# Performance work log

Measured on AMD Instinct MI355X. Metric: run time of the kernel, lower is better.

The kernel has to match this reference:

```python
import jax, jax.numpy as jnp
import numpy as np

NUM_EMBEDDINGS = 512
EMBEDDING_DIM = 64
COMMITMENT_COST = 0.25


def setup_inputs() -> dict:
    key = jax.random.key(0)
    k1, k2 = jax.random.split(key)
    inputs = jax.random.normal(k1, (128, 1024, EMBEDDING_DIM), dtype=jnp.float32)
    embedding = jax.random.normal(k2, (NUM_EMBEDDINGS, EMBEDDING_DIM), dtype=jnp.float32)
    return {"inputs": inputs, "embedding": embedding}


def reference(inputs, embedding):
    """Eval-mode forward of VectorQuantizerEMA.

    Returns (loss, quantized, perplexity, encodings), matching the torch module
    with self.training == False.
    """
    input_shape = inputs.shape
    flat = inputs.reshape(-1, EMBEDDING_DIM)                      # [N, D]
    distances = (
        jnp.sum(flat ** 2, axis=1, keepdims=True)
        + jnp.sum(embedding ** 2, axis=1)
        - 2.0 * flat @ embedding.T
    )
    encoding_indices = jnp.argmin(distances, axis=1)              # [N]
    encodings = jax.nn.one_hot(encoding_indices, NUM_EMBEDDINGS, dtype=jnp.float32)  # [N, K]
    # quantized = onehot @ W  ==  gather rows (same math, cheaper)
    quantized = jnp.take(embedding, encoding_indices, axis=0).reshape(input_shape)

    e_latent_loss = jnp.mean((jax.lax.stop_gradient(quantized) - inputs) ** 2)
    loss = COMMITMENT_COST * e_latent_loss

    # straight-through estimator
    quantized = inputs + jax.lax.stop_gradient(quantized - inputs)

    avg_probs = jnp.mean(encodings, axis=0)                       # [K]
    perplexity = jnp.exp(-jnp.sum(avg_probs * jnp.log(avg_probs + 1e-10)))
    return loss, quantized, perplexity, encodings
```

## Files before the change

### kernel.cpp

```cpp
#include <hip/hip_runtime.h>
#include <math.h>


#define NK 512
#define ND 64
#define NROWS 131072
#define ROWS_PB 64
#define BLOCK 256
#define NBLOCKS (NROWS / ROWS_PB)
#define NTILES 32
#define XSTRIDE 68
#define MARGIN 0.02f

#define Q_OFF    1
#define PERP_OFF 8388609
#define ENC_OFF  8388610

typedef float vf2 __attribute__((ext_vector_type(2)));
typedef float vf4 __attribute__((ext_vector_type(4)));
typedef short vs8 __attribute__((ext_vector_type(8)));

__device__ __forceinline__ unsigned short bf16_rne(float v) {
    union { float f; unsigned int u; } a; a.f = v;
    return (unsigned short)((a.u + 0x7FFFu + ((a.u >> 16) & 1u)) >> 16);
}
__device__ __forceinline__ float bf16_to_f(unsigned short s) {
    union { unsigned int u; float f; } a; a.u = ((unsigned int)s) << 16;
    return a.f;
}

__global__ __launch_bounds__(64) void vq_prep(const float* __restrict__ emb,
                                              float* __restrict__ eknorm,
                                              unsigned int* __restrict__ efrag) {
    const int t = blockIdx.x;
    const int l = threadIdx.x;
    const int c = t * 16 + (l & 15);
    const int quad = l >> 4;
    #pragma unroll
    for (int f = 0; f < 4; ++f) {
        const int kbase = (f & 1) * 32 + quad * 8;
        unsigned int w[4];
        #pragma unroll
        for (int d = 0; d < 4; ++d) {
            float v0 = emb[c * ND + kbase + 2 * d];
            float v1 = emb[c * ND + kbase + 2 * d + 1];
            unsigned short h0 = bf16_rne(v0), h1 = bf16_rne(v1);
            unsigned short l0 = bf16_rne(v0 - bf16_to_f(h0));
            unsigned short l1 = bf16_rne(v1 - bf16_to_f(h1));
            unsigned short e0 = (f < 2) ? h0 : l0;
            unsigned short e1 = (f < 2) ? h1 : l1;
            w[d] = (unsigned int)e0 | ((unsigned int)e1 << 16);
        }
        unsigned int* dst = efrag + ((size_t)(t * 4 + f) * 64 + l) * 4;
        dst[0] = w[0]; dst[1] = w[1]; dst[2] = w[2]; dst[3] = w[3];
    }
    if (quad == 0) {
        const vf4* er = (const vf4*)(emb + c * ND);
        float s0 = 0.f, s1 = 0.f, s2 = 0.f, s3 = 0.f;
        #pragma unroll
        for (int j = 0; j < 16; ++j) {
            vf4 v = er[j];
            s0 += v.x * v.x; s1 += v.y * v.y; s2 += v.z * v.z; s3 += v.w * v.w;
        }
        eknorm[c] = (s0 + s1) + (s2 + s3);
    }
}

__global__ __launch_bounds__(BLOCK) void vq_main(const float* __restrict__ x,
                                                 const float* __restrict__ emb,
                                                 const float* __restrict__ eknorm,
                                                 const unsigned int* __restrict__ efrag,
                                                 float* __restrict__ out,
                                                 int* __restrict__ g_counts,
                                                 float* __restrict__ g_loss) {
    __shared__ float lds_x[ROWS_PB * XSTRIDE];
    __shared__ float ek_lds[NK];
    __shared__ float d1s[ROWS_PB], d2s[ROWS_PB];
    __shared__ int   i1s[ROWS_PB], i2s[ROWS_PB];
    __shared__ int   idx_s[ROWS_PB];

    const int tid  = threadIdx.x;
    const int wave = tid >> 6;
    const int lane = tid & 63;
    const int col  = lane & 15;
    const int quad = lane >> 4;

    {
        const vf4* xp = (const vf4*)(x + (size_t)blockIdx.x * ROWS_PB * ND);
        #pragma unroll
        for (int i = 0; i < 4; ++i) {
            int e4 = tid + i * BLOCK;
            int r  = e4 >> 4;
            int c4 = (e4 & 15) * 4;
            *(vf4*)&lds_x[r * XSTRIDE + c4] = xp[e4];
        }
        ek_lds[tid] = eknorm[tid];
        ek_lds[tid + 256] = eknorm[tid + 256];
    }
    __syncthreads();

    const int arow = wave * 16 + col;
    vs8 ah0, ah1, al0, al1;
    {
        const float* xr = &lds_x[arow * XSTRIDE];
        #pragma unroll
        for (int j = 0; j < 8; ++j) {
            float va = xr[quad * 8 + j];
            float vb = xr[32 + quad * 8 + j];
            unsigned short ha = bf16_rne(va);
            unsigned short hb = bf16_rne(vb);
            ah0[j] = (short)ha; al0[j] = (short)bf16_rne(va - bf16_to_f(ha));
            ah1[j] = (short)hb; al1[j] = (short)bf16_rne(vb - bf16_to_f(hb));
        }
    }

    float d1[4], d2[4];
    int   i1[4], i2[4];
    #pragma unroll
    for (int r = 0; r < 4; ++r) { d1[r] = INFINITY; d2[r] = INFINITY; i1[r] = 0x7FFFFFFF; i2[r] = 0x7FFFFFFF; }

    const vs8* bbase = (const vs8*)efrag;
    vs8 b0 = bbase[0 * 64 + lane];
    vs8 b1 = bbase[1 * 64 + lane];
    vs8 b2 = bbase[2 * 64 + lane];
    vs8 b3 = bbase[3 * 64 + lane];

    for (int t = 0; t < NTILES; ++t) {
        vs8 n0, n1, n2, n3;
        if (t + 1 < NTILES) {
            n0 = bbase[((t + 1) * 4 + 0) * 64 + lane];
            n1 = bbase[((t + 1) * 4 + 1) * 64 + lane];
            n2 = bbase[((t + 1) * 4 + 2) * 64 + lane];
            n3 = bbase[((t + 1) * 4 + 3) * 64 + lane];
        }
        vf4 acc0 = {0.f, 0.f, 0.f, 0.f};
        vf4 acc1 = {0.f, 0.f, 0.f, 0.f};
        acc0 = __builtin_amdgcn_mfma_f32_16x16x32_bf16(ah0, b0, acc0, 0, 0, 0);
        acc1 = __builtin_amdgcn_mfma_f32_16x16x32_bf16(ah1, b1, acc1, 0, 0, 0);
        acc0 = __builtin_amdgcn_mfma_f32_16x16x32_bf16(al0, b0, acc0, 0, 0, 0);
        acc1 = __builtin_amdgcn_mfma_f32_16x16x32_bf16(al1, b1, acc1, 0, 0, 0);
        acc0 = __builtin_amdgcn_mfma_f32_16x16x32_bf16(ah0, b2, acc0, 0, 0, 0);
        acc1 = __builtin_amdgcn_mfma_f32_16x16x32_bf16(ah1, b3, acc1, 0, 0, 0);

        const float ek = ek_lds[t * 16 + col];
        const int cidx = t * 16 + col;
        #pragma unroll
        for (int r = 0; r < 4; ++r) {
            float d = ek - 2.f * (acc0[r] + acc1[r]);
            bool lt1 = d < d1[r];
            bool lt2 = d < d2[r];
            float nd2 = lt1 ? d1[r] : (lt2 ? d : d2[r]);
            int   ni2 = lt1 ? i1[r] : (lt2 ? cidx : i2[r]);
            d2[r] = nd2; i2[r] = ni2;
            d1[r] = lt1 ? d : d1[r];
            i1[r] = lt1 ? cidx : i1[r];
        }
        b0 = n0; b1 = n1; b2 = n2; b3 = n3;
    }

    #pragma unroll
    for (int m = 8; m >= 1; m >>= 1) {
        #pragma unroll
        for (int r = 0; r < 4; ++r) {
            float od1 = __shfl_xor(d1[r], m);
            int   oi1 = __shfl_xor(i1[r], m);
            float od2 = __shfl_xor(d2[r], m);
            int   oi2 = __shfl_xor(i2[r], m);
            bool aF = (d1[r] < od1) || (d1[r] == od1 && i1[r] < oi1);
            float n1 = aF ? d1[r] : od1;  int ni1 = aF ? i1[r] : oi1;
            float ca = aF ? od1 : d1[r];  int cia = aF ? oi1 : i1[r];
            float cb = aF ? d2[r] : od2;  int cib = aF ? i2[r] : oi2;
            bool bF = (cb < ca) || (cb == ca && cib < cia);
            float n2 = bF ? cb : ca;      int ni2 = bF ? cib : cia;
            d1[r] = n1; i1[r] = ni1; d2[r] = n2; i2[r] = ni2;
        }
    }
    if (col == 0) {
        #pragma unroll
        for (int r = 0; r < 4; ++r) {
            int lr = wave * 16 + quad * 4 + r;
            d1s[lr] = d1[r]; i1s[lr] = i1[r];
            d2s[lr] = d2[r]; i2s[lr] = i2[r];
        }
    }
    __syncthreads();

    if (tid < ROWS_PB) {
        int am = i1s[tid];
        float dfin = d1s[tid];
        if (d2s[tid] - dfin < MARGIN) {
            int ia = i1s[tid], ib = i2s[tid];
            const float* xr = &lds_x[tid * XSTRIDE];
            float da, db;
            {
                const vf4* er = (const vf4*)(emb + ia * ND);
                float s0 = 0.f, s1 = 0.f, s2 = 0.f, s3 = 0.f;
                #pragma unroll
                for (int j = 0; j < 16; ++j) {
                    vf4 v = er[j];
                    s0 += xr[4 * j] * v.x; s1 += xr[4 * j + 1] * v.y;
                    s2 += xr[4 * j + 2] * v.z; s3 += xr[4 * j + 3] * v.w;
                }
                da = ek_lds[ia] - 2.f * ((s0 + s1) + (s2 + s3));
            }
            {
                const vf4* er = (const vf4*)(emb + ib * ND);
                float s0 = 0.f, s1 = 0.f, s2 = 0.f, s3 = 0.f;
                #pragma unroll
                for (int j = 0; j < 16; ++j) {
                    vf4 v = er[j];
                    s0 += xr[4 * j] * v.x; s1 += xr[4 * j + 1] * v.y;
                    s2 += xr[4 * j + 2] * v.z; s3 += xr[4 * j + 3] * v.w;
                }
                db = ek_lds[ib] - 2.f * ((s0 + s1) + (s2 + s3));
            }
            bool useB = (db < da) || (db == da && ib < ia);
            am   = useB ? ib : ia;
            dfin = useB ? db : da;
        }
        idx_s[tid] = am;
        atomicAdd(&g_counts[am], 1);

        float xn;
        {
            const float* xr = &lds_x[tid * XSTRIDE];
            float s0 = 0.f, s1 = 0.f, s2 = 0.f, s3 = 0.f;
            #pragma unroll
            for (int j = 0; j < 16; ++j) {
                s0 += xr[4 * j] * xr[4 * j];         s1 += xr[4 * j + 1] * xr[4 * j + 1];
                s2 += xr[4 * j + 2] * xr[4 * j + 2]; s3 += xr[4 * j + 3] * xr[4 * j + 3];
            }
            xn = (s0 + s1) + (s2 + s3);
        }
        float lossv = xn + dfin;
        #pragma unroll
        for (int off = 32; off >= 1; off >>= 1) lossv += __shfl_down(lossv, off);
        if (tid == 0) atomicAdd(g_loss, lossv);
    }
    __syncthreads();

    float* ebase = out + ENC_OFF + (size_t)blockIdx.x * (ROWS_PB * NK);
    if (tid == 0) {
        int a0 = idx_s[0];
        vf2 h; h.x = (a0 == 0) ? 1.f : 0.f; h.y = (a0 == 1) ? 1.f : 0.f;
        *(vf2*)ebase = h;
        int a63 = idx_s[63];
        vf2 tl; tl.x = (a63 == 510) ? 1.f : 0.f; tl.y = (a63 == 511) ? 1.f : 0.f;
        *(vf2*)(ebase + ROWS_PB * NK - 2) = tl;
    }
    {
        const int c0 = (2 + 4 * tid) & 511;
        const int rb = (2 + 4 * tid) >> 9;
        if (c0 != 510) {
            #pragma unroll
            for (int i = 0; i < 32; ++i) {
                int p = tid + i * BLOCK;
                if (p < 8191) {
                    int am = idx_s[rb + 2 * i];
                    vf4 v;
                    v.x = (am == c0)     ? 1.f : 0.f;
                    v.y = (am == c0 + 1) ? 1.f : 0.f;
                    v.z = (am == c0 + 2) ? 1.f : 0.f;
                    v.w = (am == c0 + 3) ? 1.f : 0.f;
                    *(vf4*)(ebase + 2 + 4 * (size_t)p) = v;
                }
            }
        } else {
            #pragma unroll
            for (int i = 0; i < 32; ++i) {
                int p = tid + i * BLOCK;
                if (p < 8191) {
                    int r0 = rb + 2 * i;
                    int am0 = idx_s[r0];
                    int am1 = idx_s[r0 + 1];
                    vf4 v;
                    v.x = (am0 == 510) ? 1.f : 0.f;
                    v.y = (am0 == 511) ? 1.f : 0.f;
                    v.z = (am1 == 0)   ? 1.f : 0.f;
                    v.w = (am1 == 1)   ? 1.f : 0.f;
                    *(vf4*)(ebase + 2 + 4 * (size_t)p) = v;
                }
            }
        }
    }

    {
        float* qout = out + Q_OFF + (size_t)blockIdx.x * (ROWS_PB * ND);
        #pragma unroll
        for (int i = 0; i < 16; ++i) {
            int p = tid + i * BLOCK;
            qout[p] = emb[idx_s[p >> 6] * ND + (p & 63)];
        }
    }
}

__global__ __launch_bounds__(512) void vq_final(const int* __restrict__ g_counts,
                                                const float* __restrict__ g_loss,
                                                float* __restrict__ out) {
    __shared__ float red[8];
    int t = threadIdx.x;
    float p = (float)g_counts[t] * (1.0f / (float)NROWS);
    float h = p * logf(p + 1e-10f);
    #pragma unroll
    for (int off = 32; off >= 1; off >>= 1) h += __shfl_down(h, off);
    if ((t & 63) == 0) red[t >> 6] = h;
    __syncthreads();
    if (t == 0) {
        float s = 0.f;
        #pragma unroll
        for (int i = 0; i < 8; ++i) s += red[i];
        out[PERP_OFF] = expf(-s);
        out[0] = 0.25f * g_loss[0] / (float)(NROWS * ND);
    }
}

extern "C" void kernel_launch(void* const* d_in, const int* in_sizes, int n_in,
                              void* d_out, int out_size, void* d_ws, size_t ws_size,
                              hipStream_t stream) {
    const float* x   = (const float*)d_in[0];
    const float* emb = (const float*)d_in[1];
    float* out = (float*)d_out;

    int*          g_counts = (int*)d_ws;
    float*        g_loss   = (float*)((char*)d_ws + 2048);
    float*        eknorm   = (float*)((char*)d_ws + 4096);
    unsigned int* efrag    = (unsigned int*)((char*)d_ws + 8192);

    (void)hipMemsetAsync(d_ws, 0, 4096, stream);

    vq_prep<<<NTILES, 64, 0, stream>>>(emb, eknorm, efrag);
    vq_main<<<NBLOCKS, BLOCK, 0, stream>>>(x, emb, eknorm, efrag, out, g_counts, g_loss);
    vq_final<<<1, 512, 0, stream>>>(g_counts, g_loss, out);
}
```

Baseline: 387.5 us.

## Make refinement and output stages wave-local, replacing block barriers with wave barriers

After: 423.0 us. +9.2%, slower.

```diff
diff --git a/kernel.cpp b/kernel.cpp
--- a/kernel.cpp
+++ b/kernel.cpp
@@ -75,9 +75,9 @@
                                                  float* __restrict__ g_loss) {
     __shared__ float lds_x[ROWS_PB * XSTRIDE];
     __shared__ float ek_lds[NK];
-    __shared__ float d1s[ROWS_PB], d2s[ROWS_PB];
-    __shared__ int   i1s[ROWS_PB], i2s[ROWS_PB];
-    __shared__ int   idx_s[ROWS_PB];
+    __shared__ float d1w[ROWS_PB], d2w[ROWS_PB];
+    __shared__ int   i1w[ROWS_PB], i2w[ROWS_PB];
+    __shared__ int   idxw[ROWS_PB];
 
     const int tid  = threadIdx.x;
     const int wave = tid >> 6;
@@ -179,18 +179,22 @@
         #pragma unroll
         for (int r = 0; r < 4; ++r) {
             int lr = wave * 16 + quad * 4 + r;
-            d1s[lr] = d1[r]; i1s[lr] = i1[r];
-            d2s[lr] = d2[r]; i2s[lr] = i2[r];
-        }
-    }
-    __syncthreads();
-
-    if (tid < ROWS_PB) {
-        int am = i1s[tid];
-        float dfin = d1s[tid];
-        if (d2s[tid] - dfin < MARGIN) {
-            int ia = i1s[tid], ib = i2s[tid];
-            const float* xr = &lds_x[tid * XSTRIDE];
+            ((volatile float*)d1w)[lr] = d1[r];
+            ((volatile int*)  i1w)[lr] = i1[r];
+            ((volatile float*)d2w)[lr] = d2[r];
+            ((volatile int*)  i2w)[lr] = i2[r];
+        }
+    }
+    __builtin_amdgcn_wave_barrier();
+
+    if (lane < 16) {
+        const int lr = wave * 16 + lane;
+        int   am   = ((volatile int*)  i1w)[lr];
+        float dfin = ((volatile float*)d1w)[lr];
+        float dsec = ((volatile float*)d2w)[lr];
+        if (dsec - dfin < MARGIN) {
+            int ia = am, ib = ((volatile int*)i2w)[lr];
+            const float* xr = &lds_x[lr * XSTRIDE];
             float da, db;
             {
                 const vf4* er = (const vf4*)(emb + ia * ND);
@@ -218,12 +222,12 @@
             am   = useB ? ib : ia;
             dfin = useB ? db : da;
         }
-        idx_s[tid] = am;
+        ((volatile int*)idxw)[lr] = am;
         atomicAdd(&g_counts[am], 1);
 
         float xn;
         {
-            const float* xr = &lds_x[tid * XSTRIDE];
+            const float* xr = &lds_x[lr * XSTRIDE];
             float s0 = 0.f, s1 = 0.f, s2 = 0.f, s3 = 0.f;
             #pragma unroll
             for (int j = 0; j < 16; ++j) {
@@ -234,62 +238,55 @@
         }
         float lossv = xn + dfin;
         #pragma unroll
-        for (int off = 32; off >= 1; off >>= 1) lossv += __shfl_down(lossv, off);
-        if (tid == 0) atomicAdd(g_loss, lossv);
-    }
-    __syncthreads();
-
-    float* ebase = out + ENC_OFF + (size_t)blockIdx.x * (ROWS_PB * NK);
-    if (tid == 0) {
-        int a0 = idx_s[0];
+        for (int off = 8; off >= 1; off >>= 1) lossv += __shfl_down(lossv, off);
+        if (lane == 0) atomicAdd(g_loss, lossv);
+    }
+    __builtin_amdgcn_wave_barrier();
+
+    float* wenc = out + ENC_OFF + (size_t)blockIdx.x * (ROWS_PB * NK) + wave * (16 * NK);
+    if (lane == 0) {
+        int a0 = ((volatile int*)idxw)[wave * 16];
         vf2 h; h.x = (a0 == 0) ? 1.f : 0.f; h.y = (a0 == 1) ? 1.f : 0.f;
-        *(vf2*)ebase = h;
-        int a63 = idx_s[63];
-        vf2 tl; tl.x = (a63 == 510) ? 1.f : 0.f; tl.y = (a63 == 511) ? 1.f : 0.f;
-        *(vf2*)(ebase + ROWS_PB * NK - 2) = tl;
+        *(vf2*)wenc = h;
+        int a15 = ((volatile int*)idxw)[wave * 16 + 15];
+        vf2 tl; tl.x = (a15 == 510) ? 1.f : 0.f; tl.y = (a15 == 511) ? 1.f : 0.f;
+        *(vf2*)(wenc + 16 * NK - 2) = tl;
     }
     {
-        const int c0 = (2 + 4 * tid) & 511;
-        const int rb = (2 + 4 * tid) >> 9;
-        if (c0 != 510) {
-            #pragma unroll
-            for (int i = 0; i < 32; ++i) {
-                int p = tid + i * BLOCK;
-                if (p < 8191) {
-                    int am = idx_s[rb + 2 * i];
-                    vf4 v;
+        const bool crossing = (lane == 63);
+        #pragma unroll
+        for (int i = 0; i < 32; ++i) {
+            int j = lane + 64 * i;
+            if (j < 2047) {
+                int f = 2 + 4 * j;
+                int r = f >> 9;
+                int c0 = f & 511;
+                vf4 v;
+                if (crossing && (i & 1)) {
+                    int am0 = ((volatile int*)idxw)[wave * 16 + r];
+                    int am1 = ((volatile int*)idxw)[wave * 16 + r + 1];
+                    v.x = (am0 == 510) ? 1.f : 0.f;
+                    v.y = (am0 == 511) ? 1.f : 0.f;
+                    v.z = (am1 == 0)   ? 1.f : 0.f;
+                    v.w = (am1 == 1)   ? 1.f : 0.f;
+                } else {
+                    int am = ((volatile int*)idxw)[wave * 16 + r];
                     v.x = (am == c0)     ? 1.f : 0.f;
                     v.y = (am == c0 + 1) ? 1.f : 0.f;
                     v.z = (am == c0 + 2) ? 1.f : 0.f;
                     v.w = (am == c0 + 3) ? 1.f : 0.f;
-                    *(vf4*)(ebase + 2 + 4 * (size_t)p) = v;
                 }
+                *(vf4*)(wenc + f) = v;
             }
-        } else {
-            #pragma unroll
-            for (int i = 0; i < 32; ++i) {
-                int p = tid + i * BLOCK;
-                if (p < 8191) {
-                    int r0 = rb + 2 * i;
-                    int am0 = idx_s[r0];
-                    int am1 = idx_s[r0 + 1];
-                    vf4 v;
-                    v.x = (am0 == 510) ? 1.f : 0.f;
-                    v.y = (am0 == 511) ? 1.f : 0.f;
-                    v.z = (am1 == 0)   ? 1.f : 0.f;
-                    v.w = (am1 == 1)   ? 1.f : 0.f;
-                    *(vf4*)(ebase + 2 + 4 * (size_t)p) = v;
-                }
-            }
         }
     }
 
     {
-        float* qout = out + Q_OFF + (size_t)blockIdx.x * (ROWS_PB * ND);
+        float* qout = out + Q_OFF + (size_t)blockIdx.x * (ROWS_PB * ND) + wave * (16 * ND);
         #pragma unroll
         for (int i = 0; i < 16; ++i) {
-            int p = tid + i * BLOCK;
-            qout[p] = emb[idx_s[p >> 6] * ND + (p & 63)];
+            int am = ((volatile int*)idxw)[wave * 16 + i];
+            qout[i * ND + lane] = emb[am * ND + lane];
         }
     }
 }
```
